# Kernel optimization log

Hardware: AMD Instinct MI355X
Metric: run time of the kernel (lower is better)

## Reference

```python
import jax, jax.numpy as jnp
import numpy as np

D_MODEL = 1024
N_HEAD = 16
HEAD_DIM = D_MODEL // N_HEAD
B, L = 2, 2048


def setup_inputs() -> dict:
    key = jax.random.key(0)
    ks = jax.random.split(key, 5)
    std = 1.0 / np.sqrt(D_MODEL)
    x = jax.random.normal(ks[0], (B, L, D_MODEL), dtype=jnp.float32)
    # nn.MultiheadAttention packed in-projection: [3*D, D] weight, [3*D] bias
    in_proj_w = jax.random.normal(ks[1], (3 * D_MODEL, D_MODEL), dtype=jnp.float32) * std
    in_proj_b = jax.random.normal(ks[2], (3 * D_MODEL,), dtype=jnp.float32) * 0.01
    out_w = jax.random.normal(ks[3], (D_MODEL, D_MODEL), dtype=jnp.float32) * std
    out_b = jax.random.normal(ks[4], (D_MODEL,), dtype=jnp.float32) * 0.01
    return {"x": x, "in_proj_w": in_proj_w, "in_proj_b": in_proj_b,
            "out_w": out_w, "out_b": out_b}


def reference(x, in_proj_w, in_proj_b, out_w, out_b):
    b, l, d = x.shape
    h, dh = N_HEAD, HEAD_DIM
    # packed QKV projection: [B,L,3D]
    qkv = jnp.einsum('bld,ed->ble', x, in_proj_w) + in_proj_b
    q, k, v = jnp.split(qkv, 3, axis=-1)
    # [B,H,L,dh]
    q = q.reshape(b, l, h, dh).transpose(0, 2, 1, 3)
    k = k.reshape(b, l, h, dh).transpose(0, 2, 1, 3)
    v = v.reshape(b, l, h, dh).transpose(0, 2, 1, 3)
    scale = 1.0 / jnp.sqrt(jnp.asarray(dh, dtype=x.dtype))
    scores = jnp.einsum('bhqd,bhkd->bhqk', q, k) * scale  # [B,H,L,L]
    causal = jnp.tril(jnp.ones((l, l), dtype=bool))
    scores = jnp.where(causal, scores, jnp.asarray(-jnp.inf, dtype=scores.dtype))
    attn = jax.nn.softmax(scores, axis=-1)
    ctx = jnp.einsum('bhqk,bhkd->bhqd', attn, v)  # [B,H,L,dh]
    ctx = ctx.transpose(0, 2, 1, 3).reshape(b, l, d)
    out = jnp.einsum('bld,ed->ble', ctx, out_w) + out_b
    return out
```

## Files before the change

### kernel.cpp

```cpp
#include <hip/hip_runtime.h>
#include <hip/hip_bf16.h>

typedef __attribute__((ext_vector_type(8))) short short8;
typedef __attribute__((ext_vector_type(4))) short short4v;
typedef __attribute__((ext_vector_type(4))) float f32x4;

#define GAS(p) ((const __attribute__((address_space(1))) void*)(p))
#define LAS(p) ((__attribute__((address_space(3))) void*)(p))

__device__ __forceinline__ short f2bf_bits(float f) {
    __hip_bfloat16 h = __float2bfloat16(f);
    return *reinterpret_cast<short*>(&h);
}

__global__ __launch_bounds__(256) void cvt_all(const float* __restrict__ x,
                                               const float* __restrict__ w1,
                                               const float* __restrict__ w2,
                                               short* __restrict__ dx,
                                               short* __restrict__ dw1,
                                               short* __restrict__ dw2) {
    constexpr int N1 = 4194304, N2 = 3145728;
    int i = (blockIdx.x * 256 + threadIdx.x) * 8;
    const float* src; short* dst; int j;
    if (i < N1)            { src = x;  dst = dx;  j = i; }
    else if (i < N1 + N2)  { src = w1; dst = dw1; j = i - N1; }
    else                   { src = w2; dst = dw2; j = i - N1 - N2; }
    float4 a = *reinterpret_cast<const float4*>(src + j);
    float4 b = *reinterpret_cast<const float4*>(src + j + 4);
    short8 o;
    o[0] = f2bf_bits(a.x); o[1] = f2bf_bits(a.y);
    o[2] = f2bf_bits(a.z); o[3] = f2bf_bits(a.w);
    o[4] = f2bf_bits(b.x); o[5] = f2bf_bits(b.y);
    o[6] = f2bf_bits(b.z); o[7] = f2bf_bits(b.w);
    *reinterpret_cast<short8*>(dst + j) = o;
}

__global__ __launch_bounds__(256) void gemm_qkv(const __hip_bfloat16* __restrict__ A,
                                                const __hip_bfloat16* __restrict__ B,
                                                const float* __restrict__ bias,
                                                __hip_bfloat16* __restrict__ Qb,
                                                __hip_bfloat16* __restrict__ Kb,
                                                __hip_bfloat16* __restrict__ Vb) {
    constexpr int K = 1024;
    __shared__ __hip_bfloat16 smem[2][128 * 32 + 128 * 32];
    const int tid = threadIdx.x;
    const int lane = tid & 63, wid = tid >> 6;
    const int wr = wid >> 1, wc = wid & 1;
    const int lr = lane & 15, lg = lane >> 4;

    const int bid = blockIdx.x;
    const int xcd = bid & 7, w = bid >> 3;
    const int bx = (xcd & 1) * 12 + (w % 12);
    const int by = (xcd >> 1) * 8 + (w / 12);
    const int m0 = by * 128;
    const int n0 = bx * 128;

    const f32x4 fz = {0.f, 0.f, 0.f, 0.f};
    f32x4 acc[4][4];
#pragma unroll
    for (int i = 0; i < 4; i++)
#pragma unroll
        for (int j = 0; j < 4; j++) acc[i][j] = fz;

    const char* Abase = (const char*)A + (size_t)m0 * K * 2;
    const char* Bbase = (const char*)B + (size_t)n0 * K * 2;

    auto stage = [&](int buf, int kt) {
        const int kb = kt * 64;
        char* sA = (char*)&smem[buf][0];
        char* sB = (char*)&smem[buf][128 * 32];
#pragma unroll
        for (int i = 0; i < 2; i++) {
            int o = i * 4096 + tid * 16;
            int row = o >> 6, cb = o & 63;
            __builtin_amdgcn_global_load_lds(GAS(Abase + (size_t)row * 2048 + kb + cb),
                                             LAS(sA + o), 16, 0, 0);
        }
#pragma unroll
        for (int i = 0; i < 2; i++) {
            int o = i * 4096 + tid * 16;
            int row = o >> 6, cb = o & 63;
            __builtin_amdgcn_global_load_lds(GAS(Bbase + (size_t)row * 2048 + kb + cb),
                                             LAS(sB + o), 16, 0, 0);
        }
    };

    stage(0, 0);
    __syncthreads();
    int buf = 0;
    constexpr int NT = K / 32;
    for (int kt = 0; kt < NT; ++kt) {
        if (kt + 1 < NT) stage(buf ^ 1, kt + 1);
        const __hip_bfloat16* sA = &smem[buf][0];
        const __hip_bfloat16* sB = &smem[buf][128 * 32];
        short8 a[4], b[4];
#pragma unroll
        for (int i = 0; i < 4; i++)
            a[i] = *reinterpret_cast<const short8*>(sA + (wr * 64 + i * 16 + lr) * 32 + lg * 8);
#pragma unroll
        for (int j = 0; j < 4; j++)
            b[j] = *reinterpret_cast<const short8*>(sB + (wc * 64 + j * 16 + lr) * 32 + lg * 8);
#pragma unroll
        for (int i = 0; i < 4; i++)
#pragma unroll
            for (int j = 0; j < 4; j++)
                acc[i][j] = __builtin_amdgcn_mfma_f32_16x16x32_bf16(a[i], b[j], acc[i][j], 0, 0, 0);
        __syncthreads();
        buf ^= 1;
    }

#pragma unroll
    for (int j = 0; j < 4; j++) {
        int e = n0 + wc * 64 + j * 16 + lr;
        float bv = bias[e];
        int sec = e >> 10;
        int el = e & 1023;
        int h = el >> 6, d = el & 63;
        __hip_bfloat16* dst = (sec == 0) ? Qb : ((sec == 1) ? Kb : Vb);
        float scale = (sec == 0) ? 0.18033688011112042f : 1.0f;
#pragma unroll
        for (int i = 0; i < 4; i++) {
            int mb = m0 + wr * 64 + i * 16 + lg * 4;
#pragma unroll
            for (int r = 0; r < 4; r++) {
                int tok = mb + r;
                int bb = tok >> 11, l = tok & 2047;
                float v = (acc[i][j][r] + bv) * scale;
                dst[((size_t)(bb * 16 + h) * 2048 + l) * 64 + d] = __float2bfloat16(v);
            }
        }
    }
}

__global__ __launch_bounds__(256) void transpose_v(const __hip_bfloat16* __restrict__ V,
                                                   __hip_bfloat16* __restrict__ Vt) {
    __shared__ unsigned short tb[64][72];
    int bh = blockIdx.y, l0 = blockIdx.x * 64;
    int tid = threadIdx.x;
    const unsigned short* src = (const unsigned short*)V + ((size_t)bh * 2048 + l0) * 64;
#pragma unroll
    for (int i = 0; i < 2; i++) {
        int idx = i * 256 + tid;
        int row = idx >> 3;
        int c0 = (idx & 7) * 8;
        short8 v = *reinterpret_cast<const short8*>(src + row * 64 + c0);
#pragma unroll
        for (int jj = 0; jj < 8; jj++) tb[c0 + jj][row] = (unsigned short)v[jj];
    }
    __syncthreads();
    unsigned short* dst = (unsigned short*)Vt + (size_t)bh * 64 * 2048 + l0;
#pragma unroll
    for (int i = 0; i < 2; i++) {
        int idx = i * 256 + tid;
        int d = idx >> 3;
        int c8 = (idx & 7) * 8;
        short8 vv = *reinterpret_cast<const short8*>(&tb[d][c8]);
        *reinterpret_cast<short8*>(dst + (size_t)d * 2048 + c8) = vv;
    }
}

__global__ __launch_bounds__(256) void attn(const __hip_bfloat16* __restrict__ Qg,
                                            const __hip_bfloat16* __restrict__ Kg,
                                            const __hip_bfloat16* __restrict__ Vtg,
                                            __hip_bfloat16* __restrict__ ctx) {
    const int bid = blockIdx.x;
    const int xcd = bid & 7, seq = bid >> 3;
    const int bh = (xcd << 2) | (seq & 3);
    const int qt = 31 - (seq >> 2);
    const int tid = threadIdx.x, lane = tid & 63, wq = tid >> 6;
    const int lr = lane & 15, lg = lane >> 4;

    __shared__ __hip_bfloat16 Ks[2][64 * 64];
    __shared__ __hip_bfloat16 Vs[2][64 * 64];
    __shared__ __hip_bfloat16 Ps[4][16 * 72];

    const char* kbase = (const char*)Kg + (size_t)bh * (2048 * 64 * 2);
    const char* vbase = (const char*)Vtg + (size_t)bh * (64 * 2048 * 2);
    const int bb = bh >> 4, h = bh & 15;

    const int srow = tid >> 3;
    const int ssl = (tid & 7) ^ (srow & 7);
    const char* gk0 = kbase + srow * 128 + ssl * 16;
    const char* gv0 = vbase + (size_t)srow * 4096 + ssl * 16;

    const int koffA = lr * 64 + ((lg ^ (lr & 7)) * 8);
    const int koffB = lr * 64 + (((4 + lg) ^ (lr & 7)) * 8);
    __hip_bfloat16* pwW = &Ps[wq][0] + lr * 72 + lg * 4;
    const __hip_bfloat16* pwR = &Ps[wq][0] + lr * 72 + lg * 8;

    auto stage = [&](int buf, int kt) {
        char* dK = (char*)&Ks[buf][0] + tid * 16;
        char* dV = (char*)&Vs[buf][0] + tid * 16;
        const char* srcK = gk0 + (size_t)kt * 8192;
        const char* srcV = gv0 + (size_t)kt * 128;
        __builtin_amdgcn_global_load_lds(GAS(srcK), LAS(dK), 16, 0, 0);
        __builtin_amdgcn_global_load_lds(GAS(srcK + 4096), LAS(dK + 4096), 16, 0, 0);
        __builtin_amdgcn_global_load_lds(GAS(srcV), LAS(dV), 16, 0, 0);
        __builtin_amdgcn_global_load_lds(GAS(srcV + 131072), LAS(dV + 4096), 16, 0, 0);
    };

    const f32x4 fz = {0.f, 0.f, 0.f, 0.f};
    const int qb = qt * 64 + wq * 16;

    const __hip_bfloat16* Qrow = Qg + ((size_t)bh * 2048 + qb + lr) * 64 + lg * 8;
    short8 qf0 = *reinterpret_cast<const short8*>(Qrow);
    short8 qf1 = *reinterpret_cast<const short8*>(Qrow + 32);

    f32x4 o[4];
#pragma unroll
    for (int n = 0; n < 4; n++) o[n] = fz;
    float m = -1e30f, lsum = 0.f;

    const int NT = qt + 1;
    stage(0, 0);
    __syncthreads();
    int buf = 0;
    for (int kt = 0; kt < NT; ++kt) {
        if (kt + 1 < NT) stage(buf ^ 1, kt + 1);
        const __hip_bfloat16* sK = &Ks[buf][0];
        const __hip_bfloat16* sV = &Vs[buf][0];

        f32x4 s[4];
#pragma unroll
        for (int n = 0; n < 4; n++) s[n] = fz;
        __builtin_amdgcn_s_setprio(1);
#pragma unroll
        for (int n = 0; n < 4; n++) {
            short8 k0 = *reinterpret_cast<const short8*>(sK + koffA + n * 1024);
            short8 k1 = *reinterpret_cast<const short8*>(sK + koffB + n * 1024);
            s[n] = __builtin_amdgcn_mfma_f32_16x16x32_bf16(k0, qf0, s[n], 0, 0, 0);
            s[n] = __builtin_amdgcn_mfma_f32_16x16x32_bf16(k1, qf1, s[n], 0, 0, 0);
        }
        __builtin_amdgcn_s_setprio(0);

        if (kt == NT - 1) {
            int q = qb + lr;
#pragma unroll
            for (int n = 0; n < 4; n++) {
                int kvb = kt * 64 + n * 16 + lg * 4;
#pragma unroll
                for (int r = 0; r < 4; r++)
                    if (kvb + r > q) s[n][r] = -1e30f;
            }
        }

        float mx = fmaxf(fmaxf(fmaxf(s[0][0], s[0][1]), fmaxf(s[0][2], s[0][3])),
                         fmaxf(fmaxf(fmaxf(s[1][0], s[1][1]), fmaxf(s[1][2], s[1][3])),
                               fmaxf(fmaxf(fmaxf(s[2][0], s[2][1]), fmaxf(s[2][2], s[2][3])),
                                     fmaxf(fmaxf(s[3][0], s[3][1]), fmaxf(s[3][2], s[3][3])))));
        mx = fmaxf(mx, __shfl_xor(mx, 16));
        mx = fmaxf(mx, __shfl_xor(mx, 32));

        if (!__all(mx - m <= 11.54f)) {
            float mnew = fmaxf(m, mx);
            float corr = __builtin_amdgcn_exp2f(m - mnew);
            m = mnew;
            lsum *= corr;
            float c0 = __shfl(corr, (lane & 48) | (lg * 4 + 0));
            float c1 = __shfl(corr, (lane & 48) | (lg * 4 + 1));
            float c2 = __shfl(corr, (lane & 48) | (lg * 4 + 2));
            float c3 = __shfl(corr, (lane & 48) | (lg * 4 + 3));
#pragma unroll
            for (int n = 0; n < 4; n++) {
                o[n][0] *= c0; o[n][1] *= c1; o[n][2] *= c2; o[n][3] *= c3;
            }
        }

        float psum = 0.f;
#pragma unroll
        for (int n = 0; n < 4; n++) {
            float p0 = __builtin_amdgcn_exp2f(s[n][0] - m);
            float p1 = __builtin_amdgcn_exp2f(s[n][1] - m);
            float p2 = __builtin_amdgcn_exp2f(s[n][2] - m);
            float p3 = __builtin_amdgcn_exp2f(s[n][3] - m);
            s[n][0] = p0; s[n][1] = p1; s[n][2] = p2; s[n][3] = p3;
            psum += (p0 + p1) + (p2 + p3);
        }
        lsum += psum;

#pragma unroll
        for (int n = 0; n < 4; n++) {
            short4v pk;
            pk[0] = f2bf_bits(s[n][0]); pk[1] = f2bf_bits(s[n][1]);
            pk[2] = f2bf_bits(s[n][2]); pk[3] = f2bf_bits(s[n][3]);
            *reinterpret_cast<short4v*>(pwW + n * 16) = pk;
        }
        asm volatile("s_waitcnt lgkmcnt(0)" ::: "memory");
        short8 pa0 = *reinterpret_cast<const short8*>(pwR);
        short8 pa1 = *reinterpret_cast<const short8*>(pwR + 32);

        __builtin_amdgcn_s_setprio(1);
#pragma unroll
        for (int n = 0; n < 4; n++) {
            short8 vf0 = *reinterpret_cast<const short8*>(sV + koffA + n * 1024);
            short8 vf1 = *reinterpret_cast<const short8*>(sV + koffB + n * 1024);
            o[n] = __builtin_amdgcn_mfma_f32_16x16x32_bf16(pa0, vf0, o[n], 0, 0, 0);
            o[n] = __builtin_amdgcn_mfma_f32_16x16x32_bf16(pa1, vf1, o[n], 0, 0, 0);
        }
        __builtin_amdgcn_s_setprio(0);
        __syncthreads();
        buf ^= 1;
    }

    lsum += __shfl_xor(lsum, 16);
    lsum += __shfl_xor(lsum, 32);
    float l0 = __shfl(lsum, (lane & 48) | (lg * 4 + 0));
    float l1 = __shfl(lsum, (lane & 48) | (lg * 4 + 1));
    float l2 = __shfl(lsum, (lane & 48) | (lg * 4 + 2));
    float l3 = __shfl(lsum, (lane & 48) | (lg * 4 + 3));
    float inv[4] = {1.0f / l0, 1.0f / l1, 1.0f / l2, 1.0f / l3};
#pragma unroll
    for (int r = 0; r < 4; r++) {
        int tok = qb + lg * 4 + r;
        __hip_bfloat16* crow = ctx + ((size_t)(bb * 2048 + tok)) * 1024 + h * 64;
#pragma unroll
        for (int n = 0; n < 4; n++) crow[n * 16 + lr] = __float2bfloat16(o[n][r] * inv[r]);
    }
}

__global__ __launch_bounds__(256) void gemm_out(const __hip_bfloat16* __restrict__ A,
                                                const __hip_bfloat16* __restrict__ B,
                                                const float* __restrict__ bias,
                                                float* __restrict__ out) {
    constexpr int K = 1024;
    __shared__ __hip_bfloat16 smem[2][128 * 32 + 64 * 32];
    const int tid = threadIdx.x;
    const int lane = tid & 63, wid = tid >> 6;
    const int wr = wid >> 1, wc = wid & 1;
    const int lr = lane & 15, lg = lane >> 4;

    const int bid = blockIdx.x;
    const int xcd = bid & 7, w = bid >> 3;
    const int bx = w & 15;
    const int by = (xcd << 2) | (w >> 4);
    const int m0 = by * 128;
    const int n0 = bx * 64;

    const f32x4 fz = {0.f, 0.f, 0.f, 0.f};
    f32x4 acc[4][2];
#pragma unroll
    for (int i = 0; i < 4; i++)
#pragma unroll
        for (int j = 0; j < 2; j++) acc[i][j] = fz;

    const char* Abase = (const char*)A + (size_t)m0 * K * 2;
    const char* Bbase = (const char*)B + (size_t)n0 * K * 2;

    auto stage = [&](int buf, int kt) {
        const int kb = kt * 64;
        char* sA = (char*)&smem[buf][0];
        char* sB = (char*)&smem[buf][128 * 32];
#pragma unroll
        for (int i = 0; i < 2; i++) {
            int o = i * 4096 + tid * 16;
            int row = o >> 6, cb = o & 63;
            __builtin_amdgcn_global_load_lds(GAS(Abase + (size_t)row * 2048 + kb + cb),
                                             LAS(sA + o), 16, 0, 0);
        }
        {
            int o = tid * 16;
            int row = o >> 6, cb = o & 63;
            __builtin_amdgcn_global_load_lds(GAS(Bbase + (size_t)row * 2048 + kb + cb),
                                             LAS(sB + o), 16, 0, 0);
        }
    };

    stage(0, 0);
    __syncthreads();
    int buf = 0;
    constexpr int NT = K / 32;
    for (int kt = 0; kt < NT; ++kt) {
        if (kt + 1 < NT) stage(buf ^ 1, kt + 1);
        const __hip_bfloat16* sA = &smem[buf][0];
        const __hip_bfloat16* sB = &smem[buf][128 * 32];
        short8 a[4], b[2];
#pragma unroll
        for (int i = 0; i < 4; i++)
            a[i] = *reinterpret_cast<const short8*>(sA + (wr * 64 + i * 16 + lr) * 32 + lg * 8);
#pragma unroll
        for (int j = 0; j < 2; j++)
            b[j] = *reinterpret_cast<const short8*>(sB + (wc * 32 + j * 16 + lr) * 32 + lg * 8);
#pragma unroll
        for (int i = 0; i < 4; i++)
#pragma unroll
            for (int j = 0; j < 2; j++)
                acc[i][j] = __builtin_amdgcn_mfma_f32_16x16x32_bf16(a[i], b[j], acc[i][j], 0, 0, 0);
        __syncthreads();
        buf ^= 1;
    }

#pragma unroll
    for (int j = 0; j < 2; j++) {
        int e = n0 + wc * 32 + j * 16 + lr;
        float bv = bias[e];
#pragma unroll
        for (int i = 0; i < 4; i++) {
            int mb = m0 + wr * 64 + i * 16 + lg * 4;
#pragma unroll
            for (int r = 0; r < 4; r++) {
                out[(size_t)(mb + r) * 1024 + e] = acc[i][j][r] + bv;
            }
        }
    }
}

extern "C" void kernel_launch(void* const* d_in, const int* in_sizes, int n_in,
                              void* d_out, int out_size, void* d_ws, size_t ws_size,
                              hipStream_t stream) {
    const float* x = (const float*)d_in[0];
    const float* w_in = (const float*)d_in[1];
    const float* b_in = (const float*)d_in[2];
    const float* w_out = (const float*)d_in[3];
    const float* b_out = (const float*)d_in[4];
    float* out = (float*)d_out;

    char* ws = (char*)d_ws;
    __hip_bfloat16* xbf  = (__hip_bfloat16*)(ws);
    __hip_bfloat16* wbf  = (__hip_bfloat16*)(ws + (8ull << 20));
    __hip_bfloat16* owbf = (__hip_bfloat16*)(ws + (14ull << 20));
    __hip_bfloat16* Qb   = (__hip_bfloat16*)(ws + (16ull << 20));
    __hip_bfloat16* Kb   = (__hip_bfloat16*)(ws + (24ull << 20));
    __hip_bfloat16* Vb   = (__hip_bfloat16*)(ws + (32ull << 20));
    __hip_bfloat16* Vt   = (__hip_bfloat16*)(ws + (40ull << 20));
    __hip_bfloat16* ctxb = (__hip_bfloat16*)(ws + (48ull << 20));

    cvt_all<<<4096, 256, 0, stream>>>(x, w_in, w_out, (short*)xbf, (short*)wbf, (short*)owbf);
    gemm_qkv<<<768, 256, 0, stream>>>(xbf, wbf, b_in, Qb, Kb, Vb);
    transpose_v<<<dim3(32, 32), 256, 0, stream>>>(Vb, Vt);
    attn<<<1024, 256, 0, stream>>>(Qb, Kb, Vt, ctxb);
    gemm_out<<<512, 256, 0, stream>>>(ctxb, owbf, b_out, out);
}
```

Baseline: 180.6 us.

## Process two query tiles per attention block and write V transposed from QKV GEMM

```diff
diff --git a/kernel.cpp b/kernel.cpp
--- a/kernel.cpp
+++ b/kernel.cpp
@@ -40,7 +40,7 @@
                                                 const float* __restrict__ bias,
                                                 __hip_bfloat16* __restrict__ Qb,
                                                 __hip_bfloat16* __restrict__ Kb,
-                                                __hip_bfloat16* __restrict__ Vb) {
+                                                __hip_bfloat16* __restrict__ Vt) {
     constexpr int K = 1024;
     __shared__ __hip_bfloat16 smem[2][128 * 32 + 128 * 32];
     const int tid = threadIdx.x;
@@ -116,7 +116,6 @@
         int sec = e >> 10;
         int el = e & 1023;
         int h = el >> 6, d = el & 63;
-        __hip_bfloat16* dst = (sec == 0) ? Qb : ((sec == 1) ? Kb : Vb);
         float scale = (sec == 0) ? 0.18033688011112042f : 1.0f;
 #pragma unroll
         for (int i = 0; i < 4; i++) {
@@ -126,53 +125,32 @@
                 int tok = mb + r;
                 int bb = tok >> 11, l = tok & 2047;
                 float v = (acc[i][j][r] + bv) * scale;
-                dst[((size_t)(bb * 16 + h) * 2048 + l) * 64 + d] = __float2bfloat16(v);
+                __hip_bfloat16 hv = __float2bfloat16(v);
+                int bh = bb * 16 + h;
+                if (sec == 0)      Qb[((size_t)bh * 2048 + l) * 64 + d] = hv;
+                else if (sec == 1) Kb[((size_t)bh * 2048 + l) * 64 + d] = hv;
+                else               Vt[((size_t)bh * 64 + d) * 2048 + l] = hv;
             }
         }
     }
 }
 
-__global__ __launch_bounds__(256) void transpose_v(const __hip_bfloat16* __restrict__ V,
-                                                   __hip_bfloat16* __restrict__ Vt) {
-    __shared__ unsigned short tb[64][72];
-    int bh = blockIdx.y, l0 = blockIdx.x * 64;
-    int tid = threadIdx.x;
-    const unsigned short* src = (const unsigned short*)V + ((size_t)bh * 2048 + l0) * 64;
-#pragma unroll
-    for (int i = 0; i < 2; i++) {
-        int idx = i * 256 + tid;
-        int row = idx >> 3;
-        int c0 = (idx & 7) * 8;
-        short8 v = *reinterpret_cast<const short8*>(src + row * 64 + c0);
-#pragma unroll
-        for (int jj = 0; jj < 8; jj++) tb[c0 + jj][row] = (unsigned short)v[jj];
-    }
-    __syncthreads();
-    unsigned short* dst = (unsigned short*)Vt + (size_t)bh * 64 * 2048 + l0;
-#pragma unroll
-    for (int i = 0; i < 2; i++) {
-        int idx = i * 256 + tid;
-        int d = idx >> 3;
-        int c8 = (idx & 7) * 8;
-        short8 vv = *reinterpret_cast<const short8*>(&tb[d][c8]);
-        *reinterpret_cast<short8*>(dst + (size_t)d * 2048 + c8) = vv;
-    }
-}
-
-__global__ __launch_bounds__(256) void attn(const __hip_bfloat16* __restrict__ Qg,
-                                            const __hip_bfloat16* __restrict__ Kg,
-                                            const __hip_bfloat16* __restrict__ Vtg,
-                                            __hip_bfloat16* __restrict__ ctx) {
+__global__ __launch_bounds__(256, 3) void attn(const __hip_bfloat16* __restrict__ Qg,
+                                               const __hip_bfloat16* __restrict__ Kg,
+                                               const __hip_bfloat16* __restrict__ Vtg,
+                                               __hip_bfloat16* __restrict__ ctx) {
     const int bid = blockIdx.x;
     const int xcd = bid & 7, seq = bid >> 3;
     const int bh = (xcd << 2) | (seq & 3);
-    const int qt = 31 - (seq >> 2);
+    const int p = seq >> 2;
+    const int qtA = 30 - 2 * p, qtB = 31 - 2 * p;
+    const int NT = qtB + 1;
     const int tid = threadIdx.x, lane = tid & 63, wq = tid >> 6;
     const int lr = lane & 15, lg = lane >> 4;
 
-    __shared__ __hip_bfloat16 Ks[2][64 * 64];
-    __shared__ __hip_bfloat16 Vs[2][64 * 64];
-    __shared__ __hip_bfloat16 Ps[4][16 * 72];
+    __shared__ short Ks[2][64 * 64];
+    __shared__ short Vs[2][64 * 64];
+    __shared__ short Ps[2][4][16 * 64];
 
     const char* kbase = (const char*)Kg + (size_t)bh * (2048 * 64 * 2);
     const char* vbase = (const char*)Vtg + (size_t)bh * (64 * 2048 * 2);
@@ -183,10 +161,13 @@
     const char* gk0 = kbase + srow * 128 + ssl * 16;
     const char* gv0 = vbase + (size_t)srow * 4096 + ssl * 16;
 
-    const int koffA = lr * 64 + ((lg ^ (lr & 7)) * 8);
-    const int koffB = lr * 64 + (((4 + lg) ^ (lr & 7)) * 8);
-    __hip_bfloat16* pwW = &Ps[wq][0] + lr * 72 + lg * 4;
-    const __hip_bfloat16* pwR = &Ps[wq][0] + lr * 72 + lg * 8;
+    const int kfA = lr * 128 + ((lg ^ (lr & 7)) * 16);
+    const int kfB = lr * 128 + (((4 + lg) ^ (lr & 7)) * 16);
+    const int sw = (lr & 7) << 4;
+    char* pbA = (char*)&Ps[0][wq][0];
+    char* pbB = (char*)&Ps[1][wq][0];
+    const int prd0 = lr * 128 + ((lg * 16) ^ sw);
+    const int prd1 = lr * 128 + ((64 + lg * 16) ^ sw);
 
     auto stage = [&](int buf, int kt) {
         char* dK = (char*)&Ks[buf][0] + tid * 16;
@@ -199,63 +180,18 @@
         __builtin_amdgcn_global_load_lds(GAS(srcV + 131072), LAS(dV + 4096), 16, 0, 0);
     };
 
-    const f32x4 fz = {0.f, 0.f, 0.f, 0.f};
-    const int qb = qt * 64 + wq * 16;
-
-    const __hip_bfloat16* Qrow = Qg + ((size_t)bh * 2048 + qb + lr) * 64 + lg * 8;
-    short8 qf0 = *reinterpret_cast<const short8*>(Qrow);
-    short8 qf1 = *reinterpret_cast<const short8*>(Qrow + 32);
-
-    f32x4 o[4];
-#pragma unroll
-    for (int n = 0; n < 4; n++) o[n] = fz;
-    float m = -1e30f, lsum = 0.f;
-
-    const int NT = qt + 1;
-    stage(0, 0);
-    __syncthreads();
-    int buf = 0;
-    for (int kt = 0; kt < NT; ++kt) {
-        if (kt + 1 < NT) stage(buf ^ 1, kt + 1);
-        const __hip_bfloat16* sK = &Ks[buf][0];
-        const __hip_bfloat16* sV = &Vs[buf][0];
-
-        f32x4 s[4];
-#pragma unroll
-        for (int n = 0; n < 4; n++) s[n] = fz;
-        __builtin_amdgcn_s_setprio(1);
-#pragma unroll
-        for (int n = 0; n < 4; n++) {
-            short8 k0 = *reinterpret_cast<const short8*>(sK + koffA + n * 1024);
-            short8 k1 = *reinterpret_cast<const short8*>(sK + koffB + n * 1024);
-            s[n] = __builtin_amdgcn_mfma_f32_16x16x32_bf16(k0, qf0, s[n], 0, 0, 0);
-            s[n] = __builtin_amdgcn_mfma_f32_16x16x32_bf16(k1, qf1, s[n], 0, 0, 0);
-        }
-        __builtin_amdgcn_s_setprio(0);
-
-        if (kt == NT - 1) {
-            int q = qb + lr;
-#pragma unroll
-            for (int n = 0; n < 4; n++) {
-                int kvb = kt * 64 + n * 16 + lg * 4;
-#pragma unroll
-                for (int r = 0; r < 4; r++)
-                    if (kvb + r > q) s[n][r] = -1e30f;
-            }
-        }
-
+    auto smpack = [&](f32x4* s, f32x4* o, float& m, float& ls, char* pb) {
         float mx = fmaxf(fmaxf(fmaxf(s[0][0], s[0][1]), fmaxf(s[0][2], s[0][3])),
                          fmaxf(fmaxf(fmaxf(s[1][0], s[1][1]), fmaxf(s[1][2], s[1][3])),
                                fmaxf(fmaxf(fmaxf(s[2][0], s[2][1]), fmaxf(s[2][2], s[2][3])),
                                      fmaxf(fmaxf(s[3][0], s[3][1]), fmaxf(s[3][2], s[3][3])))));
         mx = fmaxf(mx, __shfl_xor(mx, 16));
         mx = fmaxf(mx, __shfl_xor(mx, 32));
-
         if (!__all(mx - m <= 11.54f)) {
             float mnew = fmaxf(m, mx);
             float corr = __builtin_amdgcn_exp2f(m - mnew);
             m = mnew;
-            lsum *= corr;
+            ls *= corr;
             float c0 = __shfl(corr, (lane & 48) | (lg * 4 + 0));
             float c1 = __shfl(corr, (lane & 48) | (lg * 4 + 1));
             float c2 = __shfl(corr, (lane & 48) | (lg * 4 + 2));
@@ -265,7 +201,6 @@
                 o[n][0] *= c0; o[n][1] *= c1; o[n][2] *= c2; o[n][3] *= c3;
             }
         }
-
         float psum = 0.f;
 #pragma unroll
         for (int n = 0; n < 4; n++) {
@@ -276,45 +211,148 @@
             s[n][0] = p0; s[n][1] = p1; s[n][2] = p2; s[n][3] = p3;
             psum += (p0 + p1) + (p2 + p3);
         }
-        lsum += psum;
-
+        ls += psum;
 #pragma unroll
         for (int n = 0; n < 4; n++) {
             short4v pk;
             pk[0] = f2bf_bits(s[n][0]); pk[1] = f2bf_bits(s[n][1]);
             pk[2] = f2bf_bits(s[n][2]); pk[3] = f2bf_bits(s[n][3]);
-            *reinterpret_cast<short4v*>(pwW + n * 16) = pk;
-        }
+            *reinterpret_cast<short4v*>(pb + lr * 128 + (((n * 32 + lg * 8) ^ sw))) = pk;
+        }
+    };
+
+    const f32x4 fz = {0.f, 0.f, 0.f, 0.f};
+    const int qbA = qtA * 64 + wq * 16;
+    const int qbB = qtB * 64 + wq * 16;
+
+    const __hip_bfloat16* QrA = Qg + ((size_t)bh * 2048 + qbA + lr) * 64 + lg * 8;
+    const __hip_bfloat16* QrB = Qg + ((size_t)bh * 2048 + qbB + lr) * 64 + lg * 8;
+    short8 qA0 = *reinterpret_cast<const short8*>(QrA);
+    short8 qA1 = *reinterpret_cast<const short8*>(QrA + 32);
+    short8 qB0 = *reinterpret_cast<const short8*>(QrB);
+    short8 qB1 = *reinterpret_cast<const short8*>(QrB + 32);
+
+    f32x4 oA[4], oB[4];
+#pragma unroll
+    for (int n = 0; n < 4; n++) { oA[n] = fz; oB[n] = fz; }
+    float mA = -1e30f, mB = -1e30f, lsA = 0.f, lsB = 0.f;
+
+    stage(0, 0);
+    __syncthreads();
+    int buf = 0;
+#pragma unroll 1
+    for (int kt = 0; kt < NT - 1; ++kt) {
+        stage(buf ^ 1, kt + 1);
+        const char* sK = (const char*)&Ks[buf][0];
+        const char* sV = (const char*)&Vs[buf][0];
+
+        f32x4 sA[4], sB[4];
+#pragma unroll
+        for (int n = 0; n < 4; n++) { sA[n] = fz; sB[n] = fz; }
+        __builtin_amdgcn_s_setprio(1);
+#pragma unroll
+        for (int n = 0; n < 4; n++) {
+            short8 k0 = *reinterpret_cast<const short8*>(sK + kfA + n * 2048);
+            short8 k1 = *reinterpret_cast<const short8*>(sK + kfB + n * 2048);
+            sB[n] = __builtin_amdgcn_mfma_f32_16x16x32_bf16(k0, qB0, sB[n], 0, 0, 0);
+            sB[n] = __builtin_amdgcn_mfma_f32_16x16x32_bf16(k1, qB1, sB[n], 0, 0, 0);
+            sA[n] = __builtin_amdgcn_mfma_f32_16x16x32_bf16(k0, qA0, sA[n], 0, 0, 0);
+            sA[n] = __builtin_amdgcn_mfma_f32_16x16x32_bf16(k1, qA1, sA[n], 0, 0, 0);
+        }
+        __builtin_amdgcn_s_setprio(0);
+
+        if (kt == NT - 2) {
+            int q = qbA + lr;
+#pragma unroll
+            for (int n = 0; n < 4; n++) {
+                int kvb = kt * 64 + n * 16 + lg * 4;
+#pragma unroll
+                for (int r = 0; r < 4; r++)
+                    if (kvb + r > q) sA[n][r] = -1e30f;
+            }
+        }
+
+        smpack(sB, oB, mB, lsB, pbB);
+        smpack(sA, oA, mA, lsA, pbA);
         asm volatile("s_waitcnt lgkmcnt(0)" ::: "memory");
-        short8 pa0 = *reinterpret_cast<const short8*>(pwR);
-        short8 pa1 = *reinterpret_cast<const short8*>(pwR + 32);
+        short8 paA0 = *reinterpret_cast<const short8*>(pbA + prd0);
+        short8 paA1 = *reinterpret_cast<const short8*>(pbA + prd1);
+        short8 paB0 = *reinterpret_cast<const short8*>(pbB + prd0);
+        short8 paB1 = *reinterpret_cast<const short8*>(pbB + prd1);
 
         __builtin_amdgcn_s_setprio(1);
 #pragma unroll
         for (int n = 0; n < 4; n++) {
-            short8 vf0 = *reinterpret_cast<const short8*>(sV + koffA + n * 1024);
-            short8 vf1 = *reinterpret_cast<const short8*>(sV + koffB + n * 1024);
-            o[n] = __builtin_amdgcn_mfma_f32_16x16x32_bf16(pa0, vf0, o[n], 0, 0, 0);
-            o[n] = __builtin_amdgcn_mfma_f32_16x16x32_bf16(pa1, vf1, o[n], 0, 0, 0);
+            short8 vf0 = *reinterpret_cast<const short8*>(sV + kfA + n * 2048);
+            short8 vf1 = *reinterpret_cast<const short8*>(sV + kfB + n * 2048);
+            oB[n] = __builtin_amdgcn_mfma_f32_16x16x32_bf16(paB0, vf0, oB[n], 0, 0, 0);
+            oB[n] = __builtin_amdgcn_mfma_f32_16x16x32_bf16(paB1, vf1, oB[n], 0, 0, 0);
+            oA[n] = __builtin_amdgcn_mfma_f32_16x16x32_bf16(paA0, vf0, oA[n], 0, 0, 0);
+            oA[n] = __builtin_amdgcn_mfma_f32_16x16x32_bf16(paA1, vf1, oA[n], 0, 0, 0);
         }
         __builtin_amdgcn_s_setprio(0);
         __syncthreads();
         buf ^= 1;
     }
 
-    lsum += __shfl_xor(lsum, 16);
-    lsum += __shfl_xor(lsum, 32);
-    float l0 = __shfl(lsum, (lane & 48) | (lg * 4 + 0));
-    float l1 = __shfl(lsum, (lane & 48) | (lg * 4 + 1));
-    float l2 = __shfl(lsum, (lane & 48) | (lg * 4 + 2));
-    float l3 = __shfl(lsum, (lane & 48) | (lg * 4 + 3));
-    float inv[4] = {1.0f / l0, 1.0f / l1, 1.0f / l2, 1.0f / l3};
-#pragma unroll
-    for (int r = 0; r < 4; r++) {
-        int tok = qb + lg * 4 + r;
-        __hip_bfloat16* crow = ctx + ((size_t)(bb * 2048 + tok)) * 1024 + h * 64;
-#pragma unroll
-        for (int n = 0; n < 4; n++) crow[n * 16 + lr] = __float2bfloat16(o[n][r] * inv[r]);
+    {
+        const int kt = NT - 1;
+        const char* sK = (const char*)&Ks[buf][0];
+        const char* sV = (const char*)&Vs[buf][0];
+        f32x4 sB[4];
+#pragma unroll
+        for (int n = 0; n < 4; n++) sB[n] = fz;
+        __builtin_amdgcn_s_setprio(1);
+#pragma unroll
+        for (int n = 0; n < 4; n++) {
+            short8 k0 = *reinterpret_cast<const short8*>(sK + kfA + n * 2048);
+            short8 k1 = *reinterpret_cast<const short8*>(sK + kfB + n * 2048);
+            sB[n] = __builtin_amdgcn_mfma_f32_16x16x32_bf16(k0, qB0, sB[n], 0, 0, 0);
+            sB[n] = __builtin_amdgcn_mfma_f32_16x16x32_bf16(k1, qB1, sB[n], 0, 0, 0);
+        }
+        __builtin_amdgcn_s_setprio(0);
+        int q = qbB + lr;
+#pragma unroll
+        for (int n = 0; n < 4; n++) {
+            int kvb = kt * 64 + n * 16 + lg * 4;
+#pragma unroll
+            for (int r = 0; r < 4; r++)
+                if (kvb + r > q) sB[n][r] = -1e30f;
+        }
+        smpack(sB, oB, mB, lsB, pbB);
+        asm volatile("s_waitcnt lgkmcnt(0)" ::: "memory");
+        short8 paB0 = *reinterpret_cast<const short8*>(pbB + prd0);
+        short8 paB1 = *reinterpret_cast<const short8*>(pbB + prd1);
+        __builtin_amdgcn_s_setprio(1);
+#pragma unroll
+        for (int n = 0; n < 4; n++) {
+            short8 vf0 = *reinterpret_cast<const short8*>(sV + kfA + n * 2048);
+            short8 vf1 = *reinterpret_cast<const short8*>(sV + kfB + n * 2048);
+            oB[n] = __builtin_amdgcn_mfma_f32_16x16x32_bf16(paB0, vf0, oB[n], 0, 0, 0);
+            oB[n] = __builtin_amdgcn_mfma_f32_16x16x32_bf16(paB1, vf1, oB[n], 0, 0, 0);
+        }
+        __builtin_amdgcn_s_setprio(0);
+    }
+
+    lsA += __shfl_xor(lsA, 16); lsA += __shfl_xor(lsA, 32);
+    lsB += __shfl_xor(lsB, 16); lsB += __shfl_xor(lsB, 32);
+#pragma unroll 1
+    for (int t = 0; t < 2; ++t) {
+        float ls = t ? lsB : lsA;
+        int qb = t ? qbB : qbA;
+        f32x4* o = t ? oB : oA;
+        float l0 = __shfl(ls, (lane & 48) | (lg * 4 + 0));
+        float l1 = __shfl(ls, (lane & 48) | (lg * 4 + 1));
+        float l2 = __shfl(ls, (lane & 48) | (lg * 4 + 2));
+        float l3 = __shfl(ls, (lane & 48) | (lg * 4 + 3));
+        float inv[4] = {1.0f / l0, 1.0f / l1, 1.0f / l2, 1.0f / l3};
+#pragma unroll
+        for (int r = 0; r < 4; r++) {
+            int tok = qb + lg * 4 + r;
+            __hip_bfloat16* crow = ctx + ((size_t)(bb * 2048 + tok)) * 1024 + h * 64;
+#pragma unroll
+            for (int n = 0; n < 4; n++) crow[n * 16 + lr] = __float2bfloat16(o[n][r] * inv[r]);
+        }
     }
 }
 
@@ -420,13 +458,11 @@
     __hip_bfloat16* owbf = (__hip_bfloat16*)(ws + (14ull << 20));
     __hip_bfloat16* Qb   = (__hip_bfloat16*)(ws + (16ull << 20));
     __hip_bfloat16* Kb   = (__hip_bfloat16*)(ws + (24ull << 20));
-    __hip_bfloat16* Vb   = (__hip_bfloat16*)(ws + (32ull << 20));
     __hip_bfloat16* Vt   = (__hip_bfloat16*)(ws + (40ull << 20));
     __hip_bfloat16* ctxb = (__hip_bfloat16*)(ws + (48ull << 20));
 
     cvt_all<<<4096, 256, 0, stream>>>(x, w_in, w_out, (short*)xbf, (short*)wbf, (short*)owbf);
-    gemm_qkv<<<768, 256, 0, stream>>>(xbf, wbf, b_in, Qb, Kb, Vb);
-    transpose_v<<<dim3(32, 32), 256, 0, stream>>>(Vb, Vt);
-    attn<<<1024, 256, 0, stream>>>(Qb, Kb, Vt, ctxb);
+    gemm_qkv<<<768, 256, 0, stream>>>(xbf, wbf, b_in, Qb, Kb, Vt);
+    attn<<<512, 256, 0, stream>>>(Qb, Kb, Vt, ctxb);
     gemm_out<<<512, 256, 0, stream>>>(ctxb, owbf, b_out, out);
 }
```

After: 194.9 us. 7.9% more time.

## Write V transposed from QKV GEMM and load K/V directly into registers in attention

Applied to the files above, without the earlier changes.

```diff
diff --git a/kernel.cpp b/kernel.cpp
--- a/kernel.cpp
+++ b/kernel.cpp
@@ -40,7 +40,7 @@
                                                 const float* __restrict__ bias,
                                                 __hip_bfloat16* __restrict__ Qb,
                                                 __hip_bfloat16* __restrict__ Kb,
-                                                __hip_bfloat16* __restrict__ Vb) {
+                                                __hip_bfloat16* __restrict__ Vt) {
     constexpr int K = 1024;
     __shared__ __hip_bfloat16 smem[2][128 * 32 + 128 * 32];
     const int tid = threadIdx.x;
@@ -116,46 +116,29 @@
         int sec = e >> 10;
         int el = e & 1023;
         int h = el >> 6, d = el & 63;
-        __hip_bfloat16* dst = (sec == 0) ? Qb : ((sec == 1) ? Kb : Vb);
         float scale = (sec == 0) ? 0.18033688011112042f : 1.0f;
 #pragma unroll
         for (int i = 0; i < 4; i++) {
             int mb = m0 + wr * 64 + i * 16 + lg * 4;
-#pragma unroll
-            for (int r = 0; r < 4; r++) {
-                int tok = mb + r;
-                int bb = tok >> 11, l = tok & 2047;
-                float v = (acc[i][j][r] + bv) * scale;
-                dst[((size_t)(bb * 16 + h) * 2048 + l) * 64 + d] = __float2bfloat16(v);
+            if (sec == 2) {
+                int bb = mb >> 11, l = mb & 2047;
+                short4v pv4;
+#pragma unroll
+                for (int r = 0; r < 4; r++) pv4[r] = f2bf_bits(acc[i][j][r] + bv);
+                *reinterpret_cast<short4v*>(&Vt[((size_t)(bb * 16 + h) * 64 + d) * 2048 + l]) = pv4;
+            } else {
+#pragma unroll
+                for (int r = 0; r < 4; r++) {
+                    int tok = mb + r;
+                    int bb = tok >> 11, l = tok & 2047;
+                    float v = (acc[i][j][r] + bv) * scale;
+                    __hip_bfloat16 hv = __float2bfloat16(v);
+                    int bh = bb * 16 + h;
+                    if (sec == 0) Qb[((size_t)bh * 2048 + l) * 64 + d] = hv;
+                    else          Kb[((size_t)bh * 2048 + l) * 64 + d] = hv;
+                }
             }
         }
-    }
-}
-
-__global__ __launch_bounds__(256) void transpose_v(const __hip_bfloat16* __restrict__ V,
-                                                   __hip_bfloat16* __restrict__ Vt) {
-    __shared__ unsigned short tb[64][72];
-    int bh = blockIdx.y, l0 = blockIdx.x * 64;
-    int tid = threadIdx.x;
-    const unsigned short* src = (const unsigned short*)V + ((size_t)bh * 2048 + l0) * 64;
-#pragma unroll
-    for (int i = 0; i < 2; i++) {
-        int idx = i * 256 + tid;
-        int row = idx >> 3;
-        int c0 = (idx & 7) * 8;
-        short8 v = *reinterpret_cast<const short8*>(src + row * 64 + c0);
-#pragma unroll
-        for (int jj = 0; jj < 8; jj++) tb[c0 + jj][row] = (unsigned short)v[jj];
-    }
-    __syncthreads();
-    unsigned short* dst = (unsigned short*)Vt + (size_t)bh * 64 * 2048 + l0;
-#pragma unroll
-    for (int i = 0; i < 2; i++) {
-        int idx = i * 256 + tid;
-        int d = idx >> 3;
-        int c8 = (idx & 7) * 8;
-        short8 vv = *reinterpret_cast<const short8*>(&tb[d][c8]);
-        *reinterpret_cast<short8*>(dst + (size_t)d * 2048 + c8) = vv;
     }
 }
 
@@ -170,55 +153,42 @@
     const int tid = threadIdx.x, lane = tid & 63, wq = tid >> 6;
     const int lr = lane & 15, lg = lane >> 4;
 
-    __shared__ __hip_bfloat16 Ks[2][64 * 64];
-    __shared__ __hip_bfloat16 Vs[2][64 * 64];
-    __shared__ __hip_bfloat16 Ps[4][16 * 72];
-
-    const char* kbase = (const char*)Kg + (size_t)bh * (2048 * 64 * 2);
-    const char* vbase = (const char*)Vtg + (size_t)bh * (64 * 2048 * 2);
+    __shared__ short Ps[4][16 * 64];
+
     const int bb = bh >> 4, h = bh & 15;
-
-    const int srow = tid >> 3;
-    const int ssl = (tid & 7) ^ (srow & 7);
-    const char* gk0 = kbase + srow * 128 + ssl * 16;
-    const char* gv0 = vbase + (size_t)srow * 4096 + ssl * 16;
-
-    const int koffA = lr * 64 + ((lg ^ (lr & 7)) * 8);
-    const int koffB = lr * 64 + (((4 + lg) ^ (lr & 7)) * 8);
-    __hip_bfloat16* pwW = &Ps[wq][0] + lr * 72 + lg * 4;
-    const __hip_bfloat16* pwR = &Ps[wq][0] + lr * 72 + lg * 8;
-
-    auto stage = [&](int buf, int kt) {
-        char* dK = (char*)&Ks[buf][0] + tid * 16;
-        char* dV = (char*)&Vs[buf][0] + tid * 16;
-        const char* srcK = gk0 + (size_t)kt * 8192;
-        const char* srcV = gv0 + (size_t)kt * 128;
-        __builtin_amdgcn_global_load_lds(GAS(srcK), LAS(dK), 16, 0, 0);
-        __builtin_amdgcn_global_load_lds(GAS(srcK + 4096), LAS(dK + 4096), 16, 0, 0);
-        __builtin_amdgcn_global_load_lds(GAS(srcV), LAS(dV), 16, 0, 0);
-        __builtin_amdgcn_global_load_lds(GAS(srcV + 131072), LAS(dV + 4096), 16, 0, 0);
-    };
-
-    const f32x4 fz = {0.f, 0.f, 0.f, 0.f};
     const int qb = qt * 64 + wq * 16;
+
+    const char* kL = (const char*)Kg + (size_t)bh * (2048 * 128) + lr * 128 + lg * 16;
+    const char* vL = (const char*)Vtg + (size_t)bh * (64 * 4096) + (size_t)lr * 4096 + lg * 16;
+
+    const int sw = (lr & 7) << 4;
+    char* pb = (char*)&Ps[wq][0];
+    char* pwW = pb + lr * 128;
+    const char* pr0 = pb + lr * 128 + ((lg * 16) ^ sw);
+    const char* pr1 = pb + lr * 128 + ((64 + lg * 16) ^ sw);
 
     const __hip_bfloat16* Qrow = Qg + ((size_t)bh * 2048 + qb + lr) * 64 + lg * 8;
     short8 qf0 = *reinterpret_cast<const short8*>(Qrow);
     short8 qf1 = *reinterpret_cast<const short8*>(Qrow + 32);
 
+    const f32x4 fz = {0.f, 0.f, 0.f, 0.f};
     f32x4 o[4];
 #pragma unroll
     for (int n = 0; n < 4; n++) o[n] = fz;
     float m = -1e30f, lsum = 0.f;
 
     const int NT = qt + 1;
-    stage(0, 0);
-    __syncthreads();
-    int buf = 0;
+#pragma unroll 1
     for (int kt = 0; kt < NT; ++kt) {
-        if (kt + 1 < NT) stage(buf ^ 1, kt + 1);
-        const __hip_bfloat16* sK = &Ks[buf][0];
-        const __hip_bfloat16* sV = &Vs[buf][0];
+        const char* kp = kL + (size_t)kt * 8192;
+        const char* vp = vL + (size_t)kt * 128;
+
+        short8 k0[4], k1[4];
+#pragma unroll
+        for (int n = 0; n < 4; n++) {
+            k0[n] = *reinterpret_cast<const short8*>(kp + n * 2048);
+            k1[n] = *reinterpret_cast<const short8*>(kp + n * 2048 + 64);
+        }
 
         f32x4 s[4];
 #pragma unroll
@@ -226,12 +196,17 @@
         __builtin_amdgcn_s_setprio(1);
 #pragma unroll
         for (int n = 0; n < 4; n++) {
-            short8 k0 = *reinterpret_cast<const short8*>(sK + koffA + n * 1024);
-            short8 k1 = *reinterpret_cast<const short8*>(sK + koffB + n * 1024);
-            s[n] = __builtin_amdgcn_mfma_f32_16x16x32_bf16(k0, qf0, s[n], 0, 0, 0);
-            s[n] = __builtin_amdgcn_mfma_f32_16x16x32_bf16(k1, qf1, s[n], 0, 0, 0);
+            s[n] = __builtin_amdgcn_mfma_f32_16x16x32_bf16(k0[n], qf0, s[n], 0, 0, 0);
+            s[n] = __builtin_amdgcn_mfma_f32_16x16x32_bf16(k1[n], qf1, s[n], 0, 0, 0);
         }
         __builtin_amdgcn_s_setprio(0);
+
+        short8 v0[4], v1[4];
+#pragma unroll
+        for (int n = 0; n < 4; n++) {
+            v0[n] = *reinterpret_cast<const short8*>(vp + (size_t)n * 65536);
+            v1[n] = *reinterpret_cast<const short8*>(vp + (size_t)n * 65536 + 64);
+        }
 
         if (kt == NT - 1) {
             int q = qb + lr;
@@ -283,23 +258,19 @@
             short4v pk;
             pk[0] = f2bf_bits(s[n][0]); pk[1] = f2bf_bits(s[n][1]);
             pk[2] = f2bf_bits(s[n][2]); pk[3] = f2bf_bits(s[n][3]);
-            *reinterpret_cast<short4v*>(pwW + n * 16) = pk;
+            *reinterpret_cast<short4v*>(pwW + ((n * 32 + lg * 8) ^ sw)) = pk;
         }
         asm volatile("s_waitcnt lgkmcnt(0)" ::: "memory");
-        short8 pa0 = *reinterpret_cast<const short8*>(pwR);
-        short8 pa1 = *reinterpret_cast<const short8*>(pwR + 32);
+        short8 pa0 = *reinterpret_cast<const short8*>(pr0);
+        short8 pa1 = *reinterpret_cast<const short8*>(pr1);
 
         __builtin_amdgcn_s_setprio(1);
 #pragma unroll
         for (int n = 0; n < 4; n++) {
-            short8 vf0 = *reinterpret_cast<const short8*>(sV + koffA + n * 1024);
-            short8 vf1 = *reinterpret_cast<const short8*>(sV + koffB + n * 1024);
-            o[n] = __builtin_amdgcn_mfma_f32_16x16x32_bf16(pa0, vf0, o[n], 0, 0, 0);
-            o[n] = __builtin_amdgcn_mfma_f32_16x16x32_bf16(pa1, vf1, o[n], 0, 0, 0);
+            o[n] = __builtin_amdgcn_mfma_f32_16x16x32_bf16(pa0, v0[n], o[n], 0, 0, 0);
+            o[n] = __builtin_amdgcn_mfma_f32_16x16x32_bf16(pa1, v1[n], o[n], 0, 0, 0);
         }
         __builtin_amdgcn_s_setprio(0);
-        __syncthreads();
-        buf ^= 1;
     }
 
     lsum += __shfl_xor(lsum, 16);
@@ -420,13 +391,11 @@
     __hip_bfloat16* owbf = (__hip_bfloat16*)(ws + (14ull << 20));
     __hip_bfloat16* Qb   = (__hip_bfloat16*)(ws + (16ull << 20));
     __hip_bfloat16* Kb   = (__hip_bfloat16*)(ws + (24ull << 20));
-    __hip_bfloat16* Vb   = (__hip_bfloat16*)(ws + (32ull << 20));
     __hip_bfloat16* Vt   = (__hip_bfloat16*)(ws + (40ull << 20));
     __hip_bfloat16* ctxb = (__hip_bfloat16*)(ws + (48ull << 20));
 
     cvt_all<<<4096, 256, 0, stream>>>(x, w_in, w_out, (short*)xbf, (short*)wbf, (short*)owbf);
-    gemm_qkv<<<768, 256, 0, stream>>>(xbf, wbf, b_in, Qb, Kb, Vb);
-    transpose_v<<<dim3(32, 32), 256, 0, stream>>>(Vb, Vt);
+    gemm_qkv<<<768, 256, 0, stream>>>(xbf, wbf, b_in, Qb, Kb, Vt);
     attn<<<1024, 256, 0, stream>>>(Qb, Kb, Vt, ctxb);
     gemm_out<<<512, 256, 0, stream>>>(ctxb, owbf, b_out, out);
 }
```

Result: slower. 278.2 us (+54.1%).
